# Performance work log

Hardware: AMD Instinct MI355X
Metric: run time of the kernel (lower is better)

## Reference

```python
import jax, jax.numpy as jnp
import numpy as np

C = 512
HEADS = 8
POOL = 4
WINDOW = 4
ALPHA = 0.7
C1 = int(C * ALPHA)   # 358
C2 = C - C1           # 154


def setup_inputs() -> dict:
    key = jax.random.key(0)
    ks = jax.random.split(key, 8)
    s = 0.02
    p = lambda k, shape: jax.random.normal(k, shape, jnp.float32) * s
    b, h, w = 8, 64, 64
    return {
        "x": jax.random.normal(ks[0], (b, C, h, w), jnp.float32),
        "h_in_w": p(ks[1], (3 * C, C)), "h_in_b": jnp.zeros((3 * C,), jnp.float32),
        "h_out_w": p(ks[2], (C, C)),    "h_out_b": jnp.zeros((C,), jnp.float32),
        "v_in_w": p(ks[3], (3 * C, C)), "v_in_b": jnp.zeros((3 * C,), jnp.float32),
        "v_out_w": p(ks[4], (C, C)),    "v_out_b": jnp.zeros((C,), jnp.float32),
        "hfc_w": p(ks[5], (C1, C)),     "hfc_b": jnp.zeros((C1,), jnp.float32),
        "vfc_w": p(ks[6], (C2, C)),     "vfc_b": jnp.zeros((C2,), jnp.float32),
    }


def _mha(q, k, v, in_w, in_b, out_w, out_b, heads):
    # q: [Lq, B, C], k/v: [Lk, B, C] (seq-first, as torch MultiheadAttention)
    Lq, B, Cd = q.shape
    D = Cd // heads
    wq, wk, wv = jnp.split(in_w, 3, axis=0)
    bq, bk, bv = jnp.split(in_b, 3, axis=0)
    qp = (q @ wq.T + bq).reshape(Lq, B, heads, D)
    kp = (k @ wk.T + bk).reshape(k.shape[0], B, heads, D)
    vp = (v @ wv.T + bv).reshape(v.shape[0], B, heads, D)
    scale = 1.0 / (D ** 0.5)
    scores = jnp.einsum('qbhd,kbhd->bhqk', qp * scale, kp)
    a = jax.nn.softmax(scores, axis=-1)
    o = jnp.einsum('bhqk,kbhd->qbhd', a, vp).reshape(Lq, B, Cd)
    return o @ out_w.T + out_b


def _forward(x, h_in_w, h_in_b, h_out_w, h_out_b,
             v_in_w, v_in_b, v_out_w, v_out_b,
             hfc_w, hfc_b, vfc_w, vfc_b):
    b, c, h, w = x.shape
    # ---- horizontal attention: full-res Q, avg-pooled K,V ----
    q = x.reshape(b, c, h * w).transpose(2, 0, 1)                 # [h*w, b, c]
    xp = x.reshape(b, c, h // POOL, POOL, w // POOL, POOL).mean((3, 5))
    kv = xp.reshape(b, c, -1).transpose(2, 0, 1)                  # [(h/P)*(w/P), b, c]
    ha_x = _mha(q, kv, kv, h_in_w, h_in_b, h_out_w, h_out_b, HEADS)  # [h*w, b, c]
    ha = ha_x @ hfc_w.T + hfc_b                                   # [h*w, b, c1]
    # ---- vertical attention: independent attention per width window ----
    nw = w // WINDOW
    # (b,c,h,nw,wd) -> (h,wd,b,nw,c) -> [h*wd, b*nw, c]; batched over windows
    xv = x.reshape(b, c, h, nw, WINDOW).transpose(2, 4, 0, 3, 1).reshape(h * WINDOW, b * nw, c)
    vo = _mha(xv, xv, xv, v_in_w, v_in_b, v_out_w, v_out_b, HEADS)
    # back to (h, w, b, c) with w = nw*WINDOW block order as in the torch cat loop
    va_x = vo.reshape(h, WINDOW, b, nw, c).transpose(0, 3, 1, 2, 4).reshape(h * w, b, c)
    va = va_x @ vfc_w.T + vfc_b                                   # [h*w, b, c2]
    # ---- concat + residual + layer_norm over (c,h,w) ----
    attn = jnp.concatenate([ha, va], axis=2)                      # [h*w, b, c]
    attn_bchw = attn.reshape(h, w, b, c).transpose(2, 3, 0, 1)    # [b, c, h, w]
    res = attn_bchw + x
    mu = res.mean((1, 2, 3), keepdims=True)
    var = ((res - mu) ** 2).mean((1, 2, 3), keepdims=True)
    result = (res - mu) / jnp.sqrt(var + 1e-5)
    return (result,
            ha_x.reshape(h, w, b, c),
            va_x.reshape(h, w, b, c),
            attn_bchw)


def reference(x, h_in_w, h_in_b, h_out_w, h_out_b,
              v_in_w, v_in_b, v_out_w, v_out_b,
              hfc_w, hfc_b, vfc_w, vfc_b):
    return _forward(x, h_in_w, h_in_b, h_out_w, h_out_b,
                    v_in_w, v_in_b, v_out_w, v_out_b,
                    hfc_w, hfc_b, vfc_w, vfc_b)
```

## Files before the change

kernel.cpp:

```cpp
#include <hip/hip_runtime.h>
#include <cstdint>
#include <cstddef>

#define CD    512
#define HD    64
#define C1D   358
#define C2D   154
#define BB    8
#define PP    4096
#define NT    32768
#define LKK   256

typedef __attribute__((ext_vector_type(8))) short bf16x8;
typedef __attribute__((ext_vector_type(4))) float f32x4;

__device__ __forceinline__ unsigned short f2bf(float f) {
    union { float f; unsigned u; } v; v.f = f;
    unsigned r = v.u + 0x7FFF + ((v.u >> 16) & 1);
    return (unsigned short)(r >> 16);
}
__device__ __forceinline__ float bf2f(unsigned short s) {
    union { unsigned u; float f; } v; v.u = ((unsigned)s) << 16;
    return v.f;
}

#define GL_LDS16(gp, lp) __builtin_amdgcn_global_load_lds( \
    (const __attribute__((address_space(1))) unsigned int*)(gp), \
    (__attribute__((address_space(3))) unsigned int*)(lp), 16, 0, 0)

__global__ __launch_bounds__(256)
void cast_w(const float* __restrict__ src, unsigned short* __restrict__ dst, int n) {
    int i = blockIdx.x * 256 + threadIdx.x;
    if (i < n) dst[i] = f2bf(src[i]);
}

__global__ __launch_bounds__(256)
void pad_w(const float* __restrict__ src, unsigned short* __restrict__ dst,
           int Nreal, int Npad, int K) {
    int i = blockIdx.x * 256 + threadIdx.x;
    if (i < Npad * K) {
        int r = i / K, c = i - r * K;
        dst[i] = (r < Nreal) ? f2bf(src[(size_t)r * K + c]) : 0;
    }
}

__global__ __launch_bounds__(256)
void transpose_x(const float* __restrict__ x, unsigned short* __restrict__ Xt) {
    __shared__ float tile[32][33];
    const int b  = blockIdx.z;
    const int p0 = blockIdx.x << 5;
    const int c0 = blockIdx.y << 5;
    const int tx = threadIdx.x;
    const int ty = threadIdx.y;
#pragma unroll
    for (int i = 0; i < 4; i++) {
        int c = c0 + ty + (i << 3);
        tile[ty + (i << 3)][tx] = x[((size_t)b * CD + c) * PP + p0 + tx];
    }
    __syncthreads();
#pragma unroll
    for (int i = 0; i < 4; i++) {
        int p = p0 + ty + (i << 3);
        Xt[((size_t)p * BB + b) * CD + c0 + tx] = f2bf(tile[tx][ty + (i << 3)]);
    }
}

__global__ __launch_bounds__(256)
void make_xv(const float* __restrict__ x, unsigned short* __restrict__ Xv) {
    __shared__ float tile[32][33];
    const int b  = blockIdx.z;
    const int p0 = blockIdx.x << 5;
    const int c0 = blockIdx.y << 5;
    const int tx = threadIdx.x;
    const int ty = threadIdx.y;
#pragma unroll
    for (int i = 0; i < 4; i++) {
        int c = c0 + ty + (i << 3);
        tile[ty + (i << 3)][tx] = x[((size_t)b * CD + c) * PP + p0 + tx];
    }
    __syncthreads();
#pragma unroll
    for (int i = 0; i < 4; i++) {
        int p  = p0 + ty + (i << 3);
        int c  = c0 + tx;
        int hh = p >> 6, ww = p & 63;
        int nw = ww >> 2, wd = ww & 3;
        int tp = ((hh << 2) + wd) * 128 + (b << 4) + nw;
        Xv[(size_t)tp * CD + c] = f2bf(tile[tx][ty + (i << 3)]);
    }
}

__global__ __launch_bounds__(512)
void pool_from_xt(const unsigned short* __restrict__ Xt, unsigned short* __restrict__ Xp) {
    const int u = blockIdx.x;
    const int c = threadIdx.x;
    const int b = u >> 8, k = u & 255;
    const int ph = k >> 4, pw = k & 15;
    float s = 0.f;
#pragma unroll
    for (int dy = 0; dy < 4; dy++)
#pragma unroll
        for (int dx = 0; dx < 4; dx++) {
            int p = ((ph << 2) + dy) * 64 + (pw << 2) + dx;
            s += bf2f(Xt[((size_t)p * BB + b) * CD + c]);
        }
    Xp[(size_t)u * CD + c] = f2bf(s * (1.f / 16.f));
}

__device__ __forceinline__ void stage_tile(const unsigned short* __restrict__ g,
                                           unsigned short* l, int K, int tid) {
#pragma unroll
    for (int i = 0; i < 4; i++) {
        int c  = i * 256 + tid;
        int r  = c >> 3;
        int ko = (c & 7) << 3;
        GL_LDS16(g + (size_t)r * K + ko, l + c * 8);
    }
}

__global__ __launch_bounds__(256)
void gemm_mfma(const unsigned short* __restrict__ A, const unsigned short* __restrict__ W,
               const float* __restrict__ bias,
               float* __restrict__ Cf, unsigned short* __restrict__ Cb,
               int M, int K, int Nreal) {
    __shared__ unsigned short ldsA[2][128][64];
    __shared__ unsigned short ldsB[2][128][64];
    const int tid  = threadIdx.x;
    const int lane = tid & 63;
    const int wid  = tid >> 6;
    const int wr = wid >> 1, wc = wid & 1;
    const int lr = lane & 15, lg = lane >> 4;
    const int row0 = blockIdx.y << 7;
    const int col0 = blockIdx.x << 7;

    f32x4 zero = {0.f, 0.f, 0.f, 0.f};
    f32x4 acc[4][4];
#pragma unroll
    for (int m = 0; m < 4; m++)
#pragma unroll
        for (int n = 0; n < 4; n++) acc[m][n] = zero;

    const unsigned short* Ab = A + (size_t)row0 * K;
    const unsigned short* Wb = W + (size_t)col0 * K;

    stage_tile(Ab, &ldsA[0][0][0], K, tid);
    stage_tile(Wb, &ldsB[0][0][0], K, tid);
    __syncthreads();

    const int NTILES = K >> 6;
    int buf = 0;
    for (int t = 0; t < NTILES; t++) {
        if (t + 1 < NTILES) {
            stage_tile(Ab + ((t + 1) << 6), &ldsA[buf ^ 1][0][0], K, tid);
            stage_tile(Wb + ((t + 1) << 6), &ldsB[buf ^ 1][0][0], K, tid);
        }
#pragma unroll
        for (int kk = 0; kk < 2; kk++) {
            bf16x8 af[4], bfr[4];
#pragma unroll
            for (int m = 0; m < 4; m++)
                af[m] = *reinterpret_cast<const bf16x8*>(&ldsA[buf][wr * 64 + m * 16 + lr][kk * 32 + lg * 8]);
#pragma unroll
            for (int n = 0; n < 4; n++)
                bfr[n] = *reinterpret_cast<const bf16x8*>(&ldsB[buf][wc * 64 + n * 16 + lr][kk * 32 + lg * 8]);
#pragma unroll
            for (int m = 0; m < 4; m++)
#pragma unroll
                for (int n = 0; n < 4; n++)
                    acc[m][n] = __builtin_amdgcn_mfma_f32_16x16x32_bf16(af[m], bfr[n], acc[m][n], 0, 0, 0);
        }
        __syncthreads();
        buf ^= 1;
    }

#pragma unroll
    for (int n = 0; n < 4; n++) {
        int col = col0 + wc * 64 + n * 16 + lr;
        bool cok = col < Nreal;
        float bv = cok ? bias[col] : 0.f;
#pragma unroll
        for (int m = 0; m < 4; m++) {
            int row = row0 + wr * 64 + m * 16 + lg * 4;
            if (cok) {
#pragma unroll
                for (int i = 0; i < 4; i++) {
                    float v = acc[m][n][i] + bv;
                    if (Cf) Cf[(size_t)(row + i) * Nreal + col] = v;
                    if (Cb) Cb[(size_t)(row + i) * Nreal + col] = f2bf(v);
                }
            }
        }
    }
}

__global__ __launch_bounds__(512)
void attn_mfma(const unsigned short* __restrict__ Q, const unsigned short* __restrict__ Kp,
               const unsigned short* __restrict__ Vp, unsigned short* __restrict__ O,
               int QT, int QB, int KT, int KB) {
    __shared__ unsigned short Kb[256][72];
    __shared__ unsigned short Vt[64][264];
    __shared__ unsigned short Pl[8][16][264];
    const int tid  = threadIdx.x;
    const int lane = tid & 63;
    const int w    = tid >> 6;
    const int lr = lane & 15, lg = lane >> 4;
    const int bh = blockIdx.y, bi = bh >> 3, h = bh & 7;
    const int q0 = blockIdx.x << 7;

    for (int idx = tid; idx < 8192; idx += 512) {
        int k  = idx >> 5;
        int d2 = (idx & 31) << 1;
        size_t grow = ((size_t)k * KT + (size_t)bi * KB) * CD + h * HD + d2;
        unsigned int kv = *reinterpret_cast<const unsigned int*>(&Kp[grow]);
        unsigned int vv = *reinterpret_cast<const unsigned int*>(&Vp[grow]);
        Kb[k][d2]     = (unsigned short)(kv & 0xffff);
        Kb[k][d2 + 1] = (unsigned short)(kv >> 16);
        Vt[d2][k]     = (unsigned short)(vv & 0xffff);
        Vt[d2 + 1][k] = (unsigned short)(vv >> 16);
    }
    __syncthreads();

    const int qrow = q0 + w * 16 + lr;
    const size_t qbase = ((size_t)qrow * QT + (size_t)bi * QB) * CD + h * HD;
    bf16x8 qf0 = *reinterpret_cast<const bf16x8*>(&Q[qbase + lg * 8]);
    bf16x8 qf1 = *reinterpret_cast<const bf16x8*>(&Q[qbase + 32 + lg * 8]);

    f32x4 zero = {0.f, 0.f, 0.f, 0.f};
    f32x4 sacc[16];
#pragma unroll
    for (int t = 0; t < 16; t++) sacc[t] = zero;
#pragma unroll
    for (int t = 0; t < 16; t++) {
        bf16x8 kb0 = *reinterpret_cast<const bf16x8*>(&Kb[t * 16 + lr][lg * 8]);
        bf16x8 kb1 = *reinterpret_cast<const bf16x8*>(&Kb[t * 16 + lr][32 + lg * 8]);
        sacc[t] = __builtin_amdgcn_mfma_f32_16x16x32_bf16(qf0, kb0, sacc[t], 0, 0, 0);
        sacc[t] = __builtin_amdgcn_mfma_f32_16x16x32_bf16(qf1, kb1, sacc[t], 0, 0, 0);
    }
#pragma unroll
    for (int t = 0; t < 16; t++) sacc[t] = sacc[t] * 0.125f;

    float mrow[4] = {-1e30f, -1e30f, -1e30f, -1e30f};
#pragma unroll
    for (int t = 0; t < 16; t++)
#pragma unroll
        for (int i = 0; i < 4; i++) mrow[i] = fmaxf(mrow[i], sacc[t][i]);
#pragma unroll
    for (int i = 0; i < 4; i++) {
        mrow[i] = fmaxf(mrow[i], __shfl_xor(mrow[i], 1));
        mrow[i] = fmaxf(mrow[i], __shfl_xor(mrow[i], 2));
        mrow[i] = fmaxf(mrow[i], __shfl_xor(mrow[i], 4));
        mrow[i] = fmaxf(mrow[i], __shfl_xor(mrow[i], 8));
    }
    float ssum[4] = {0.f, 0.f, 0.f, 0.f};
#pragma unroll
    for (int t = 0; t < 16; t++)
#pragma unroll
        for (int i = 0; i < 4; i++) {
            float p = __expf(sacc[t][i] - mrow[i]);
            sacc[t][i] = p;
            ssum[i] += p;
        }
#pragma unroll
    for (int i = 0; i < 4; i++) {
        ssum[i] += __shfl_xor(ssum[i], 1);
        ssum[i] += __shfl_xor(ssum[i], 2);
        ssum[i] += __shfl_xor(ssum[i], 4);
        ssum[i] += __shfl_xor(ssum[i], 8);
    }
    float rinv[4];
#pragma unroll
    for (int i = 0; i < 4; i++) rinv[i] = 1.f / ssum[i];

#pragma unroll
    for (int t = 0; t < 16; t++)
#pragma unroll
        for (int i = 0; i < 4; i++)
            Pl[w][lg * 4 + i][t * 16 + lr] = f2bf(sacc[t][i] * rinv[i]);

    f32x4 oacc[4];
#pragma unroll
    for (int n = 0; n < 4; n++) oacc[n] = zero;
#pragma unroll
    for (int ks = 0; ks < 8; ks++) {
        bf16x8 pa = *reinterpret_cast<const bf16x8*>(&Pl[w][lr][ks * 32 + lg * 8]);
#pragma unroll
        for (int n = 0; n < 4; n++) {
            bf16x8 vb = *reinterpret_cast<const bf16x8*>(&Vt[n * 16 + lr][ks * 32 + lg * 8]);
            oacc[n] = __builtin_amdgcn_mfma_f32_16x16x32_bf16(pa, vb, oacc[n], 0, 0, 0);
        }
    }
#pragma unroll
    for (int n = 0; n < 4; n++)
#pragma unroll
        for (int i = 0; i < 4; i++) {
            int qr2 = q0 + w * 16 + lg * 4 + i;
            size_t ob = ((size_t)qr2 * QT + (size_t)bi * QB) * CD + h * HD + n * 16 + lr;
            O[ob] = f2bf(oacc[n][i]);
        }
}

__global__ __launch_bounds__(512)
void permute_va(const float* __restrict__ VOX, float* __restrict__ vax,
                unsigned short* __restrict__ vaxb) {
    const int t = blockIdx.x;
    const int c = threadIdx.x;
    const int p = t >> 3, b = t & 7;
    const int hh = p >> 6, ww = p & 63;
    const int nw = ww >> 2, wd = ww & 3;
    const int tp = ((hh << 2) + wd) * 128 + (b << 4) + nw;
    float v = VOX[(size_t)tp * CD + c];
    vax[(size_t)t * CD + c]  = v;
    vaxb[(size_t)t * CD + c] = f2bf(v);
}

__global__ __launch_bounds__(256)
void concat_stats(const float* __restrict__ HA, const float* __restrict__ VA,
                  const float* __restrict__ x, float* __restrict__ attn_out,
                  float* __restrict__ PS, float* __restrict__ PQ) {
    __shared__ float tile[32][33];
    __shared__ float wsum[4], wsq[4];
    const int b  = blockIdx.z;
    const int c0 = blockIdx.y << 5;
    const int tx = threadIdx.x;
    const int ty = threadIdx.y;
    const int tl = ty * 32 + tx;
    float lsum = 0.f, lsq = 0.f;

    for (int s = 0; s < 4; s++) {
        const int p0 = ((blockIdx.x << 2) + s) << 5;
#pragma unroll
        for (int i = 0; i < 4; i++) {
            int c = c0 + tx;
            int p = p0 + ty + (i << 3);
            size_t t = (size_t)p * BB + b;
            float v = (c < C1D) ? HA[t * C1D + c] : VA[t * C2D + (c - C1D)];
            tile[ty + (i << 3)][tx] = v;
        }
        __syncthreads();
#pragma unroll
        for (int i = 0; i < 4; i++) {
            int c = c0 + ty + (i << 3);
            int p = p0 + tx;
            size_t o = ((size_t)b * CD + c) * PP + p;
            float v = tile[tx][ty + (i << 3)];
            attn_out[o] = v;
            float r = v + x[o];
            lsum += r; lsq += r * r;
        }
        __syncthreads();
    }

    for (int off = 32; off; off >>= 1) {
        lsum += __shfl_xor(lsum, off);
        lsq  += __shfl_xor(lsq, off);
    }
    if ((tl & 63) == 0) { wsum[tl >> 6] = lsum; wsq[tl >> 6] = lsq; }
    __syncthreads();
    if (tl == 0) {
        const int bid = blockIdx.z * 512 + blockIdx.y * 32 + blockIdx.x;
        PS[bid] = wsum[0] + wsum[1] + wsum[2] + wsum[3];
        PQ[bid] = wsq[0] + wsq[1] + wsq[2] + wsq[3];
    }
}

__global__ __launch_bounds__(512)
void stats_final2(const float* __restrict__ PS, const float* __restrict__ PQ,
                  float* __restrict__ stats) {
    const int w    = threadIdx.x >> 6;
    const int lane = threadIdx.x & 63;
    float s = 0.f, q = 0.f;
    for (int i = lane; i < 512; i += 64) {
        s += PS[w * 512 + i];
        q += PQ[w * 512 + i];
    }
    for (int off = 32; off; off >>= 1) {
        s += __shfl_xor(s, off);
        q += __shfl_xor(q, off);
    }
    if (lane == 0) {
        const float n = (float)CD * (float)PP;
        float mu  = s / n;
        float var = q / n - mu * mu;
        stats[16 + w] = mu;
        stats[24 + w] = 1.f / sqrtf(var + 1e-5f);
    }
}

__global__ __launch_bounds__(256)
void norm_kernel(const float* __restrict__ attn, const float* __restrict__ x,
                 const float* __restrict__ stats, float* __restrict__ out) {
    size_t i = ((size_t)blockIdx.x * blockDim.x + threadIdx.x) * 4;
    int b = (int)(i >> 21);
    float mu  = stats[16 + b];
    float inv = stats[24 + b];
    const float4 a4 = *reinterpret_cast<const float4*>(attn + i);
    const float4 x4 = *reinterpret_cast<const float4*>(x + i);
    float4 r;
    r.x = (a4.x + x4.x - mu) * inv;
    r.y = (a4.y + x4.y - mu) * inv;
    r.z = (a4.z + x4.z - mu) * inv;
    r.w = (a4.w + x4.w - mu) * inv;
    *reinterpret_cast<float4*>(out + i) = r;
}

extern "C" void kernel_launch(void* const* d_in, const int* in_sizes, int n_in,
                              void* d_out, int out_size, void* d_ws, size_t ws_size,
                              hipStream_t stream) {
    const float* x     = (const float*)d_in[0];
    const float* hinw  = (const float*)d_in[1];
    const float* hinb  = (const float*)d_in[2];
    const float* houtw = (const float*)d_in[3];
    const float* houtb = (const float*)d_in[4];
    const float* vinw  = (const float*)d_in[5];
    const float* vinb  = (const float*)d_in[6];
    const float* voutw = (const float*)d_in[7];
    const float* voutb = (const float*)d_in[8];
    const float* hfcw  = (const float*)d_in[9];
    const float* hfcb  = (const float*)d_in[10];
    const float* vfcw  = (const float*)d_in[11];
    const float* vfcb  = (const float*)d_in[12];

    char* wsb = (char*)d_ws;
    unsigned short* R0  = (unsigned short*)(wsb);
    unsigned short* R1  = (unsigned short*)(wsb + 33554432);
    unsigned short* R2  = (unsigned short*)(wsb + 67108864);
    unsigned short* R3  = (unsigned short*)(wsb + 100663296);
    unsigned short* XP  = (unsigned short*)(wsb + 134217728);
    unsigned short* KHb = (unsigned short*)(wsb + 136314880);
    unsigned short* VHb = (unsigned short*)(wsb + 138412032);
    float* HA = (float*)(wsb + 140509184);
    float* VA = (float*)(wsb + 187432960);
    unsigned short* Whin  = (unsigned short*)(wsb + 207618048);
    unsigned short* Whout = Whin + 786432;
    unsigned short* Wvin  = Whout + 262144;
    unsigned short* Wvout = Wvin + 786432;
    unsigned short* Whfc  = Wvout + 262144;
    unsigned short* Wvfc  = Whfc + 196608;
    float* STATS = (float*)(wsb + 212467712);
    float* PS    = (float*)(wsb + 212471808);
    float* PQ    = PS + 4096;

    float* out_res = (float*)d_out;
    float* out_hax = out_res + 16777216;
    float* out_vax = out_res + 33554432;
    float* out_att = out_res + 50331648;

    cast_w<<<3072, 256, 0, stream>>>(hinw,  Whin,  786432);
    cast_w<<<1024, 256, 0, stream>>>(houtw, Whout, 262144);
    cast_w<<<3072, 256, 0, stream>>>(vinw,  Wvin,  786432);
    cast_w<<<1024, 256, 0, stream>>>(voutw, Wvout, 262144);
    pad_w<<<768, 256, 0, stream>>>(hfcw, Whfc, C1D, 384, CD);
    pad_w<<<512, 256, 0, stream>>>(vfcw, Wvfc, C2D, 256, CD);

    const dim3 tb(32, 8, 1);
    const dim3 tgrid(128, 16, 8);

    transpose_x<<<tgrid, tb, 0, stream>>>(x, R0);
    pool_from_xt<<<2048, 512, 0, stream>>>(R0, XP);
    gemm_mfma<<<dim3(4, 256), 256, 0, stream>>>(R0, Whin, hinb, nullptr, R1, NT, CD, CD);
    gemm_mfma<<<dim3(4, 16), 256, 0, stream>>>(XP, Whin + 262144, hinb + CD, nullptr, KHb, 2048, CD, CD);
    gemm_mfma<<<dim3(4, 16), 256, 0, stream>>>(XP, Whin + 524288, hinb + 2 * CD, nullptr, VHb, 2048, CD, CD);
    attn_mfma<<<dim3(32, 64), 512, 0, stream>>>(R1, KHb, VHb, R1, BB, 1, 1, 256);
    gemm_mfma<<<dim3(4, 256), 256, 0, stream>>>(R1, Whout, houtb, out_hax, R0, NT, CD, CD);
    gemm_mfma<<<dim3(3, 256), 256, 0, stream>>>(R0, Whfc, hfcb, HA, nullptr, NT, CD, C1D);

    make_xv<<<tgrid, tb, 0, stream>>>(x, R2);
    gemm_mfma<<<dim3(4, 256), 256, 0, stream>>>(R2, Wvin, vinb, nullptr, R1, NT, CD, CD);
    gemm_mfma<<<dim3(4, 256), 256, 0, stream>>>(R2, Wvin + 262144, vinb + CD, nullptr, R0, NT, CD, CD);
    gemm_mfma<<<dim3(4, 256), 256, 0, stream>>>(R2, Wvin + 524288, vinb + 2 * CD, nullptr, R3, NT, CD, CD);
    attn_mfma<<<dim3(2, 1024), 512, 0, stream>>>(R1, R0, R3, R1, 128, 1, 128, 1);
    gemm_mfma<<<dim3(4, 256), 256, 0, stream>>>(R1, Wvout, voutb, out_att, nullptr, NT, CD, CD);
    permute_va<<<NT, 512, 0, stream>>>(out_att, out_vax, R2);
    gemm_mfma<<<dim3(2, 256), 256, 0, stream>>>(R2, Wvfc, vfcb, VA, nullptr, NT, CD, C2D);

    concat_stats<<<dim3(32, 16, 8), tb, 0, stream>>>(HA, VA, x, out_att, PS, PQ);
    stats_final2<<<1, 512, 0, stream>>>(PS, PQ, STATS);
    norm_kernel<<<16384, 256, 0, stream>>>(out_att, x, STATS, out_res);
}
```

Baseline: 958.8 us.

## Fuse weight casts, input transposes, QKV projections and output permutation into fewer kernels

```diff
diff --git a/kernel.cpp b/kernel.cpp
--- a/kernel.cpp
+++ b/kernel.cpp
@@ -29,23 +29,36 @@
     (__attribute__((address_space(3))) unsigned int*)(lp), 16, 0, 0)
 
 __global__ __launch_bounds__(256)
-void cast_w(const float* __restrict__ src, unsigned short* __restrict__ dst, int n) {
+void cast_all(const float* __restrict__ hinw, const float* __restrict__ houtw,
+              const float* __restrict__ vinw, const float* __restrict__ voutw,
+              const float* __restrict__ hfcw, const float* __restrict__ vfcw,
+              unsigned short* __restrict__ Whin, unsigned short* __restrict__ Whout,
+              unsigned short* __restrict__ Wvin, unsigned short* __restrict__ Wvout,
+              unsigned short* __restrict__ Whfc, unsigned short* __restrict__ Wvfc) {
     int i = blockIdx.x * 256 + threadIdx.x;
-    if (i < n) dst[i] = f2bf(src[i]);
-}
-
-__global__ __launch_bounds__(256)
-void pad_w(const float* __restrict__ src, unsigned short* __restrict__ dst,
-           int Nreal, int Npad, int K) {
-    int i = blockIdx.x * 256 + threadIdx.x;
-    if (i < Npad * K) {
-        int r = i / K, c = i - r * K;
-        dst[i] = (r < Nreal) ? f2bf(src[(size_t)r * K + c]) : 0;
-    }
-}
-
-__global__ __launch_bounds__(256)
-void transpose_x(const float* __restrict__ x, unsigned short* __restrict__ Xt) {
+    if (i < 786432) { Whin[i] = f2bf(hinw[i]); return; }
+    i -= 786432;
+    if (i < 262144) { Whout[i] = f2bf(houtw[i]); return; }
+    i -= 262144;
+    if (i < 786432) { Wvin[i] = f2bf(vinw[i]); return; }
+    i -= 786432;
+    if (i < 262144) { Wvout[i] = f2bf(voutw[i]); return; }
+    i -= 262144;
+    if (i < 196608) {
+        int r = i >> 9, c = i & 511;
+        Whfc[i] = (r < C1D) ? f2bf(hfcw[r * CD + c]) : 0;
+        return;
+    }
+    i -= 196608;
+    {
+        int r = i >> 9, c = i & 511;
+        Wvfc[i] = (r < C2D) ? f2bf(vfcw[r * CD + c]) : 0;
+    }
+}
+
+__global__ __launch_bounds__(256)
+void transpose_both(const float* __restrict__ x, unsigned short* __restrict__ Xt,
+                    unsigned short* __restrict__ Xv) {
     __shared__ float tile[32][33];
     const int b  = blockIdx.z;
     const int p0 = blockIdx.x << 5;
@@ -60,33 +73,14 @@
     __syncthreads();
 #pragma unroll
     for (int i = 0; i < 4; i++) {
-        int p = p0 + ty + (i << 3);
-        Xt[((size_t)p * BB + b) * CD + c0 + tx] = f2bf(tile[tx][ty + (i << 3)]);
-    }
-}
-
-__global__ __launch_bounds__(256)
-void make_xv(const float* __restrict__ x, unsigned short* __restrict__ Xv) {
-    __shared__ float tile[32][33];
-    const int b  = blockIdx.z;
-    const int p0 = blockIdx.x << 5;
-    const int c0 = blockIdx.y << 5;
-    const int tx = threadIdx.x;
-    const int ty = threadIdx.y;
-#pragma unroll
-    for (int i = 0; i < 4; i++) {
-        int c = c0 + ty + (i << 3);
-        tile[ty + (i << 3)][tx] = x[((size_t)b * CD + c) * PP + p0 + tx];
-    }
-    __syncthreads();
-#pragma unroll
-    for (int i = 0; i < 4; i++) {
         int p  = p0 + ty + (i << 3);
         int c  = c0 + tx;
+        unsigned short v = f2bf(tile[tx][ty + (i << 3)]);
+        Xt[((size_t)p * BB + b) * CD + c] = v;
         int hh = p >> 6, ww = p & 63;
         int nw = ww >> 2, wd = ww & 3;
         int tp = ((hh << 2) + wd) * 128 + (b << 4) + nw;
-        Xv[(size_t)tp * CD + c] = f2bf(tile[tx][ty + (i << 3)]);
+        Xv[(size_t)tp * CD + c] = v;
     }
 }
 
@@ -118,6 +112,58 @@
     }
 }
 
+__device__ __forceinline__ void gemm_core(const unsigned short* __restrict__ A,
+                                          const unsigned short* __restrict__ W,
+                                          int K, int row0, int col0, int tid,
+                                          unsigned short* ldsA, unsigned short* ldsB,
+                                          f32x4 acc[4][4]) {
+    const int lane = tid & 63;
+    const int wid  = tid >> 6;
+    const int wr = wid >> 1, wc = wid & 1;
+    const int lr = lane & 15, lg = lane >> 4;
+
+    f32x4 zero = {0.f, 0.f, 0.f, 0.f};
+#pragma unroll
+    for (int m = 0; m < 4; m++)
+#pragma unroll
+        for (int n = 0; n < 4; n++) acc[m][n] = zero;
+
+    const unsigned short* Ab = A + (size_t)row0 * K;
+    const unsigned short* Wb = W + (size_t)col0 * K;
+
+    stage_tile(Ab, ldsA, K, tid);
+    stage_tile(Wb, ldsB, K, tid);
+    __syncthreads();
+
+    const int NTILES = K >> 6;
+    int buf = 0;
+    for (int t = 0; t < NTILES; t++) {
+        if (t + 1 < NTILES) {
+            stage_tile(Ab + ((t + 1) << 6), ldsA + ((buf ^ 1) << 13), K, tid);
+            stage_tile(Wb + ((t + 1) << 6), ldsB + ((buf ^ 1) << 13), K, tid);
+        }
+#pragma unroll
+        for (int kk = 0; kk < 2; kk++) {
+            bf16x8 af[4], bfr[4];
+#pragma unroll
+            for (int m = 0; m < 4; m++)
+                af[m] = *reinterpret_cast<const bf16x8*>(
+                    ldsA + (buf << 13) + (wr * 64 + m * 16 + lr) * 64 + kk * 32 + lg * 8);
+#pragma unroll
+            for (int n = 0; n < 4; n++)
+                bfr[n] = *reinterpret_cast<const bf16x8*>(
+                    ldsB + (buf << 13) + (wc * 64 + n * 16 + lr) * 64 + kk * 32 + lg * 8);
+#pragma unroll
+            for (int m = 0; m < 4; m++)
+#pragma unroll
+                for (int n = 0; n < 4; n++)
+                    acc[m][n] = __builtin_amdgcn_mfma_f32_16x16x32_bf16(af[m], bfr[n], acc[m][n], 0, 0, 0);
+        }
+        __syncthreads();
+        buf ^= 1;
+    }
+}
+
 __global__ __launch_bounds__(256)
 void gemm_mfma(const unsigned short* __restrict__ A, const unsigned short* __restrict__ W,
                const float* __restrict__ bias,
@@ -125,53 +171,14 @@
                int M, int K, int Nreal) {
     __shared__ unsigned short ldsA[2][128][64];
     __shared__ unsigned short ldsB[2][128][64];
-    const int tid  = threadIdx.x;
-    const int lane = tid & 63;
-    const int wid  = tid >> 6;
+    const int tid = threadIdx.x;
+    const int lane = tid & 63, wid = tid >> 6;
     const int wr = wid >> 1, wc = wid & 1;
     const int lr = lane & 15, lg = lane >> 4;
     const int row0 = blockIdx.y << 7;
     const int col0 = blockIdx.x << 7;
-
-    f32x4 zero = {0.f, 0.f, 0.f, 0.f};
     f32x4 acc[4][4];
-#pragma unroll
-    for (int m = 0; m < 4; m++)
-#pragma unroll
-        for (int n = 0; n < 4; n++) acc[m][n] = zero;
-
-    const unsigned short* Ab = A + (size_t)row0 * K;
-    const unsigned short* Wb = W + (size_t)col0 * K;
-
-    stage_tile(Ab, &ldsA[0][0][0], K, tid);
-    stage_tile(Wb, &ldsB[0][0][0], K, tid);
-    __syncthreads();
-
-    const int NTILES = K >> 6;
-    int buf = 0;
-    for (int t = 0; t < NTILES; t++) {
-        if (t + 1 < NTILES) {
-            stage_tile(Ab + ((t + 1) << 6), &ldsA[buf ^ 1][0][0], K, tid);
-            stage_tile(Wb + ((t + 1) << 6), &ldsB[buf ^ 1][0][0], K, tid);
-        }
-#pragma unroll
-        for (int kk = 0; kk < 2; kk++) {
-            bf16x8 af[4], bfr[4];
-#pragma unroll
-            for (int m = 0; m < 4; m++)
-                af[m] = *reinterpret_cast<const bf16x8*>(&ldsA[buf][wr * 64 + m * 16 + lr][kk * 32 + lg * 8]);
-#pragma unroll
-            for (int n = 0; n < 4; n++)
-                bfr[n] = *reinterpret_cast<const bf16x8*>(&ldsB[buf][wc * 64 + n * 16 + lr][kk * 32 + lg * 8]);
-#pragma unroll
-            for (int m = 0; m < 4; m++)
-#pragma unroll
-                for (int n = 0; n < 4; n++)
-                    acc[m][n] = __builtin_amdgcn_mfma_f32_16x16x32_bf16(af[m], bfr[n], acc[m][n], 0, 0, 0);
-        }
-        __syncthreads();
-        buf ^= 1;
-    }
+    gemm_core(A, W, K, row0, col0, tid, &ldsA[0][0][0], &ldsB[0][0][0], acc);
 
 #pragma unroll
     for (int n = 0; n < 4; n++) {
@@ -188,6 +195,75 @@
                     if (Cf) Cf[(size_t)(row + i) * Nreal + col] = v;
                     if (Cb) Cb[(size_t)(row + i) * Nreal + col] = f2bf(v);
                 }
+            }
+        }
+    }
+}
+
+__global__ __launch_bounds__(256)
+void gemm_mfma_seg(const unsigned short* __restrict__ A, const unsigned short* __restrict__ W,
+                   const float* __restrict__ bias,
+                   unsigned short* __restrict__ D0, unsigned short* __restrict__ D1,
+                   unsigned short* __restrict__ D2, int M, int K) {
+    __shared__ unsigned short ldsA[2][128][64];
+    __shared__ unsigned short ldsB[2][128][64];
+    const int tid = threadIdx.x;
+    const int lane = tid & 63, wid = tid >> 6;
+    const int wr = wid >> 1, wc = wid & 1;
+    const int lr = lane & 15, lg = lane >> 4;
+    const int row0 = blockIdx.y << 7;
+    const int col0 = blockIdx.x << 7;
+    f32x4 acc[4][4];
+    gemm_core(A, W, K, row0, col0, tid, &ldsA[0][0][0], &ldsB[0][0][0], acc);
+
+#pragma unroll
+    for (int n = 0; n < 4; n++) {
+        int col = col0 + wc * 64 + n * 16 + lr;
+        int seg = col >> 9, c2 = col & 511;
+        unsigned short* dst = (seg == 0) ? D0 : ((seg == 1) ? D1 : D2);
+        float bv = bias[col];
+#pragma unroll
+        for (int m = 0; m < 4; m++) {
+            int row = row0 + wr * 64 + m * 16 + lg * 4;
+#pragma unroll
+            for (int i = 0; i < 4; i++)
+                dst[(size_t)(row + i) * CD + c2] = f2bf(acc[m][n][i] + bv);
+        }
+    }
+}
+
+__global__ __launch_bounds__(256)
+void gemm_mfma_vperm(const unsigned short* __restrict__ A, const unsigned short* __restrict__ W,
+                     const float* __restrict__ bias,
+                     float* __restrict__ Cf, unsigned short* __restrict__ Cb, int K) {
+    __shared__ unsigned short ldsA[2][128][64];
+    __shared__ unsigned short ldsB[2][128][64];
+    const int tid = threadIdx.x;
+    const int lane = tid & 63, wid = tid >> 6;
+    const int wr = wid >> 1, wc = wid & 1;
+    const int lr = lane & 15, lg = lane >> 4;
+    const int row0 = blockIdx.y << 7;
+    const int col0 = blockIdx.x << 7;
+    f32x4 acc[4][4];
+    gemm_core(A, W, K, row0, col0, tid, &ldsA[0][0][0], &ldsB[0][0][0], acc);
+
+#pragma unroll
+    for (int n = 0; n < 4; n++) {
+        int col = col0 + wc * 64 + n * 16 + lr;
+        float bv = bias[col];
+#pragma unroll
+        for (int m = 0; m < 4; m++) {
+            int rbase = row0 + wr * 64 + m * 16 + lg * 4;
+#pragma unroll
+            for (int i = 0; i < 4; i++) {
+                int r = rbase + i;
+                int s = r >> 7, rem = r & 127;
+                int b = rem >> 4, nw = rem & 15;
+                int hh = s >> 2, wd = s & 3;
+                int t = (((hh << 6) + (nw << 2) + wd) << 3) + b;
+                float v = acc[m][n][i] + bv;
+                Cf[(size_t)t * CD + col] = v;
+                Cb[(size_t)t * CD + col] = f2bf(v);
             }
         }
     }
@@ -297,20 +373,6 @@
             size_t ob = ((size_t)qr2 * QT + (size_t)bi * QB) * CD + h * HD + n * 16 + lr;
             O[ob] = f2bf(oacc[n][i]);
         }
-}
-
-__global__ __launch_bounds__(512)
-void permute_va(const float* __restrict__ VOX, float* __restrict__ vax,
-                unsigned short* __restrict__ vaxb) {
-    const int t = blockIdx.x;
-    const int c = threadIdx.x;
-    const int p = t >> 3, b = t & 7;
-    const int hh = p >> 6, ww = p & 63;
-    const int nw = ww >> 2, wd = ww & 3;
-    const int tp = ((hh << 2) + wd) * 128 + (b << 4) + nw;
-    float v = VOX[(size_t)tp * CD + c];
-    vax[(size_t)t * CD + c]  = v;
-    vaxb[(size_t)t * CD + c] = f2bf(v);
 }
 
 __global__ __launch_bounds__(256)
@@ -445,32 +507,24 @@
     float* out_vax = out_res + 33554432;
     float* out_att = out_res + 50331648;
 
-    cast_w<<<3072, 256, 0, stream>>>(hinw,  Whin,  786432);
-    cast_w<<<1024, 256, 0, stream>>>(houtw, Whout, 262144);
-    cast_w<<<3072, 256, 0, stream>>>(vinw,  Wvin,  786432);
-    cast_w<<<1024, 256, 0, stream>>>(voutw, Wvout, 262144);
-    pad_w<<<768, 256, 0, stream>>>(hfcw, Whfc, C1D, 384, CD);
-    pad_w<<<512, 256, 0, stream>>>(vfcw, Wvfc, C2D, 256, CD);
+    cast_all<<<9472, 256, 0, stream>>>(hinw, houtw, vinw, voutw, hfcw, vfcw,
+                                       Whin, Whout, Wvin, Wvout, Whfc, Wvfc);
 
     const dim3 tb(32, 8, 1);
-    const dim3 tgrid(128, 16, 8);
-
-    transpose_x<<<tgrid, tb, 0, stream>>>(x, R0);
+
+    transpose_both<<<dim3(128, 16, 8), tb, 0, stream>>>(x, R0, R2);
     pool_from_xt<<<2048, 512, 0, stream>>>(R0, XP);
+
     gemm_mfma<<<dim3(4, 256), 256, 0, stream>>>(R0, Whin, hinb, nullptr, R1, NT, CD, CD);
-    gemm_mfma<<<dim3(4, 16), 256, 0, stream>>>(XP, Whin + 262144, hinb + CD, nullptr, KHb, 2048, CD, CD);
-    gemm_mfma<<<dim3(4, 16), 256, 0, stream>>>(XP, Whin + 524288, hinb + 2 * CD, nullptr, VHb, 2048, CD, CD);
+    gemm_mfma_seg<<<dim3(8, 16), 256, 0, stream>>>(XP, Whin + 262144, hinb + 512,
+                                                   KHb, VHb, nullptr, 2048, CD);
     attn_mfma<<<dim3(32, 64), 512, 0, stream>>>(R1, KHb, VHb, R1, BB, 1, 1, 256);
     gemm_mfma<<<dim3(4, 256), 256, 0, stream>>>(R1, Whout, houtb, out_hax, R0, NT, CD, CD);
     gemm_mfma<<<dim3(3, 256), 256, 0, stream>>>(R0, Whfc, hfcb, HA, nullptr, NT, CD, C1D);
 
-    make_xv<<<tgrid, tb, 0, stream>>>(x, R2);
-    gemm_mfma<<<dim3(4, 256), 256, 0, stream>>>(R2, Wvin, vinb, nullptr, R1, NT, CD, CD);
-    gemm_mfma<<<dim3(4, 256), 256, 0, stream>>>(R2, Wvin + 262144, vinb + CD, nullptr, R0, NT, CD, CD);
-    gemm_mfma<<<dim3(4, 256), 256, 0, stream>>>(R2, Wvin + 524288, vinb + 2 * CD, nullptr, R3, NT, CD, CD);
+    gemm_mfma_seg<<<dim3(12, 256), 256, 0, stream>>>(R2, Wvin, vinb, R1, R0, R3, NT, CD);
     attn_mfma<<<dim3(2, 1024), 512, 0, stream>>>(R1, R0, R3, R1, 128, 1, 128, 1);
-    gemm_mfma<<<dim3(4, 256), 256, 0, stream>>>(R1, Wvout, voutb, out_att, nullptr, NT, CD, CD);
-    permute_va<<<NT, 512, 0, stream>>>(out_att, out_vax, R2);
+    gemm_mfma_vperm<<<dim3(4, 256), 256, 0, stream>>>(R1, Wvout, voutb, out_vax, R2, CD);
     gemm_mfma<<<dim3(2, 256), 256, 0, stream>>>(R2, Wvfc, vfcb, VA, nullptr, NT, CD, C2D);
 
     concat_stats<<<dim3(32, 16, 8), tb, 0, stream>>>(HA, VA, x, out_att, PS, PQ);
```

Result: faster. 846.1 us (-11.8%).
